# Kernel optimization log

Measured on AMD Instinct MI355X. Metric: run time of the kernel, lower is better.

## Reference

```python
import jax, jax.numpy as jnp
import numpy as np

B, I, O, S, C = 64, 2048, 2048, 10, 512  # batch, input, output, dendritic segments, context dim


def setup_inputs() -> dict:
    key = jax.random.key(0)
    ks = jax.random.split(key, 8)
    x = jax.random.normal(ks[0], (B, I), dtype=jnp.float32)
    context = jax.random.normal(ks[1], (B, C), dtype=jnp.float32)
    prev_activation = jax.random.normal(ks[2], (B, I), dtype=jnp.float32)
    # sparse-initialized weight: randn/sqrt(I) * (rand > sparsity)
    w = jax.random.normal(ks[3], (O, I), dtype=jnp.float32) / np.sqrt(I)
    mask = (jax.random.uniform(ks[4], (O, I)) > 0.9).astype(jnp.float32)
    weight = w * mask
    bias = jnp.zeros((O,), dtype=jnp.float32)
    astrocyte_activation = jnp.ones((O,), dtype=jnp.float32)
    astrocyte_threshold = jnp.full((O,), 0.5, dtype=jnp.float32)
    dendrite_segments = jax.random.normal(ks[5], (O, I, S), dtype=jnp.float32) / np.sqrt(I)
    dendritic_gates = jnp.ones((O, S), dtype=jnp.float32)
    connection_strength = jnp.ones((O, I), dtype=jnp.float32)
    pruning_threshold = jnp.full((1,), 0.01, dtype=jnp.float32)
    return {
        "x": x, "context": context, "prev_activation": prev_activation,
        "weight": weight, "bias": bias,
        "astrocyte_activation": astrocyte_activation,
        "astrocyte_threshold": astrocyte_threshold,
        "dendrite_segments": dendrite_segments,
        "dendritic_gates": dendritic_gates,
        "connection_strength": connection_strength,
        "pruning_threshold": pruning_threshold,
    }


def reference(x, context, prev_activation, weight, bias, astrocyte_activation,
              astrocyte_threshold, dendrite_segments, dendritic_gates,
              connection_strength, pruning_threshold):
    dt = x.dtype
    # structural plasticity (eval branch): prune weak connections
    conn_mask = (jnp.abs(weight) * connection_strength > pruning_threshold[0]).astype(dt)
    eff_w = weight * conn_mask  # [O, I]
    # astrocyte modulation
    ctx_signal = jnp.mean(context, axis=-1, keepdims=True)          # [B, 1]
    astro = jax.nn.sigmoid(ctx_signal * astrocyte_activation[None, :])  # [B, O]
    astro = astro * (astro > astrocyte_threshold[None, :]).astype(dt)
    mean_astro = jnp.mean(astro, axis=0)                            # [O]
    mod_w = eff_w * mean_astro[:, None]                             # [O, I]
    synaptic = x @ mod_w.T + bias                                   # [B, O]
    # multi-compartment dendritic processing
    seg_act = jnp.einsum('bi,ois->bos', x, dendrite_segments)       # [B, O, S]
    gated = jax.nn.relu(seg_act) * jax.nn.sigmoid(dendritic_gates)[None, :, :]
    dendritic = jnp.sum(gated, axis=-1)                             # [B, O]
    return jax.nn.relu(synaptic + dendritic)
```

## Files before the change

kernel.cpp:

```cpp
#include <hip/hip_runtime.h>
#include <math.h>

#define Bn 64
#define In 2048
#define On 2048
#define Sn 10
#define Cn 512

#define OT 4
#define KSPLIT 4
#define KRANGE (In / KSPLIT)
#define KT 128
#define NSTG (KRANGE / KT)
#define LROW 136
#define SLOT 12

typedef short short8 __attribute__((ext_vector_type(8)));
typedef float f32x4 __attribute__((ext_vector_type(4)));
typedef unsigned short ushort4v __attribute__((ext_vector_type(4)));

__device__ __forceinline__ unsigned short f2bf(float f) {
    union { float f; unsigned u; } v; v.f = f;
    unsigned r = (v.u + 0x7FFFu + ((v.u >> 16) & 1u)) >> 16;
    return (unsigned short)r;
}

__global__ void prep_kernel(const float* __restrict__ x,
                            const float* __restrict__ ctx,
                            float* __restrict__ ws_ctx,
                            unsigned short* __restrict__ ws_xbf) {
    const int b = blockIdx.x;
    const int t = threadIdx.x;
    if (b < Bn) {
        __shared__ float red[256];
        red[t] = ctx[b * Cn + t] + ctx[b * Cn + t + 256];
        __syncthreads();
        for (int off = 128; off > 0; off >>= 1) {
            if (t < off) red[t] += red[t + off];
            __syncthreads();
        }
        if (t == 0) ws_ctx[b] = red[0] * (1.0f / (float)Cn);
    } else {
        int idx = (b - Bn) * 256 + t;
        ws_xbf[idx] = f2bf(x[idx]);
    }
}

__global__ void mastro_kernel(const float* __restrict__ aact,
                              const float* __restrict__ athr,
                              const float* __restrict__ ws_ctx,
                              float* __restrict__ ws_mastro) {
    const int o = blockIdx.x * 256 + threadIdx.x;
    const float aa = aact[o], th = athr[o];
    float sum = 0.0f;
    for (int b = 0; b < Bn; ++b) {
        float sg = 1.0f / (1.0f + expf(-ws_ctx[b] * aa));
        if (sg > th) sum += sg;
    }
    ws_mastro[o] = sum * (1.0f / (float)Bn);
}

__global__ __launch_bounds__(256, 8)
void main_kernel(const unsigned short* __restrict__ xbf,
                 const float* __restrict__ wgt,
                 const float* __restrict__ cst,
                 const float* __restrict__ seg,
                 const float* __restrict__ prn,
                 float* __restrict__ P) {
    __shared__ __align__(16) unsigned short Blds[48 * LROW];

    const int t = threadIdx.x;
    const int grp = blockIdx.x >> 2;
    const int ks  = blockIdx.x & 3;
    const int o0 = grp * OT;
    const int ib = ks * KRANGE;
    const int w = t >> 6, l = t & 63;
    const int l15 = l & 15, q = l >> 4;
    const float pthr = prn[0];

    for (int idx = t; idx < 4 * LROW; idx += 256) Blds[44 * LROW + idx] = 0;

    f32x4 acc[3];
#pragma unroll
    for (int n = 0; n < 3; ++n) acc[n] = (f32x4){0.f, 0.f, 0.f, 0.f};

    const float* segw = seg + ((size_t)(o0 + w) * In) * Sn;

    for (int is = 0; is < NSTG; ++is) {
        const int i0 = ib + is * KT;

        unsigned psv[10];
        {
            const float* sp = segw + (size_t)i0 * Sn;
#pragma unroll
            for (int c = 0; c < 10; ++c) {
                float2 f2 = *(const float2*)(sp + c * 128 + 2 * l);
                psv[c] = (unsigned)f2bf(f2.x) | ((unsigned)f2bf(f2.y) << 16);
            }
        }
        ushort4v ew[2];
        if (w == 0) {
#pragma unroll
            for (int i = 0; i < 2; ++i) {
                const int o_l = i * 2 + (l >> 5);
                const int col = (l & 31) * 4;
                f32x4 wv = *(const f32x4*)(wgt + (size_t)(o0 + o_l) * In + i0 + col);
                f32x4 cv = *(const f32x4*)(cst + (size_t)(o0 + o_l) * In + i0 + col);
#pragma unroll
                for (int j = 0; j < 4; ++j) {
                    float wj = wv[j];
                    ew[i][j] = f2bf((__builtin_fabsf(wj) * cv[j] > pthr) ? wj : 0.0f);
                }
            }
        }

        __syncthreads();

#pragma unroll
        for (int c = 0; c < 10; ++c) {
            unsigned j = (unsigned)(c * 128 + 2 * l);
            unsigned ii = j / 10u;
            unsigned s = j - ii * 10u;
            unsigned short* bp = &Blds[(w * Sn + s) * LROW + ii];
            bp[0] = (unsigned short)psv[c];
            bp[LROW] = (unsigned short)(psv[c] >> 16);
        }
        if (w == 0) {
#pragma unroll
            for (int i = 0; i < 2; ++i) {
                const int o_l = i * 2 + (l >> 5);
                const int col = (l & 31) * 4;
                *(ushort4v*)&Blds[(40 + o_l) * LROW + col] = ew[i];
            }
        }
        __syncthreads();

        const unsigned short* xrow = xbf + (size_t)(w * 16 + l15) * In + i0 + q * 8;
#pragma unroll
        for (int kk = 0; kk < KT; kk += 32) {
            short8 a  = *(const short8*)(xrow + kk);
            short8 b0 = *(const short8*)&Blds[(0  + l15) * LROW + q * 8 + kk];
            short8 b1 = *(const short8*)&Blds[(16 + l15) * LROW + q * 8 + kk];
            short8 b2 = *(const short8*)&Blds[(32 + l15) * LROW + q * 8 + kk];
            acc[0] = __builtin_amdgcn_mfma_f32_16x16x32_bf16(a, b0, acc[0], 0, 0, 0);
            acc[1] = __builtin_amdgcn_mfma_f32_16x16x32_bf16(a, b1, acc[1], 0, 0, 0);
            acc[2] = __builtin_amdgcn_mfma_f32_16x16x32_bf16(a, b2, acc[2], 0, 0, 0);
        }
    }

#pragma unroll
    for (int nt = 0; nt < 3; ++nt) {
        const unsigned n = nt * 16 + l15;
#pragma unroll
        for (int r = 0; r < 4; ++r) {
            const int m = w * 16 + q * 4 + r;
            const size_t base = (((size_t)ks * Bn + m) * On + o0) * SLOT;
            if (n < 40u) {
                unsigned ol = n / 10u, s = n - ol * 10u;
                P[base + ol * SLOT + s] = acc[nt][r];
            } else if (n < 44u) {
                P[base + (n - 40u) * SLOT + 10] = acc[nt][r];
            }
        }
    }
}

__global__ void finalize_kernel(const float* __restrict__ P,
                                const float* __restrict__ gates,
                                const float* __restrict__ bias,
                                const float* __restrict__ ws_mastro,
                                float* __restrict__ out) {
    const int t = threadIdx.x;
    const int o = (blockIdx.x & 31) * 64 + (t & 63);
    const int b = (blockIdx.x >> 5) * 4 + (t >> 6);
    f32x4 v0 = {0.f, 0.f, 0.f, 0.f}, v1 = v0, v2 = v0;
#pragma unroll
    for (int ks = 0; ks < KSPLIT; ++ks) {
        const f32x4* p = (const f32x4*)(P + (((size_t)ks * Bn + b) * On + o) * SLOT);
        v0 += p[0]; v1 += p[1]; v2 += p[2];
    }
    float d[12];
#pragma unroll
    for (int j = 0; j < 4; ++j) { d[j] = v0[j]; d[4 + j] = v1[j]; d[8 + j] = v2[j]; }
    float dend = 0.0f;
#pragma unroll
    for (int s = 0; s < Sn; ++s) {
        float g = 1.0f / (1.0f + expf(-gates[o * Sn + s]));
        float r = d[s] > 0.0f ? d[s] : 0.0f;
        dend += r * g;
    }
    float val = d[10] * ws_mastro[o] + bias[o] + dend;
    out[(size_t)b * On + o] = val > 0.0f ? val : 0.0f;
}

extern "C" void kernel_launch(void* const* d_in, const int* in_sizes, int n_in,
                              void* d_out, int out_size, void* d_ws, size_t ws_size,
                              hipStream_t stream) {
    (void)in_sizes; (void)n_in; (void)out_size; (void)ws_size;
    const float* x    = (const float*)d_in[0];
    const float* ctx  = (const float*)d_in[1];
    const float* wgt  = (const float*)d_in[3];
    const float* bias = (const float*)d_in[4];
    const float* aact = (const float*)d_in[5];
    const float* athr = (const float*)d_in[6];
    const float* seg  = (const float*)d_in[7];
    const float* gat  = (const float*)d_in[8];
    const float* cst  = (const float*)d_in[9];
    const float* prn  = (const float*)d_in[10];
    float* out = (float*)d_out;

    float* ws_ctx = (float*)d_ws;
    unsigned short* ws_xbf = (unsigned short*)((char*)d_ws + 256);
    float* ws_mastro = (float*)((char*)d_ws + 262400);
    float* ws_P = (float*)((char*)d_ws + 270592);

    prep_kernel<<<Bn + (Bn * In) / 256, 256, 0, stream>>>(x, ctx, ws_ctx, ws_xbf);
    mastro_kernel<<<On / 256, 256, 0, stream>>>(aact, athr, ws_ctx, ws_mastro);
    main_kernel<<<(On / OT) * KSPLIT, 256, 0, stream>>>(ws_xbf, wgt, cst, seg, prn, ws_P);
    finalize_kernel<<<(On / 64) * (Bn / 4), 256, 0, stream>>>(ws_P, gat, bias, ws_mastro, out);
}
```

Baseline: 312.2 us.

## Double-buffer LDS stages with smaller K tile and vectorize partial-sum stores

Halves the K tile and double-buffers the shared-memory B tile so global loads for the next stage are issued while the current stage's MFMAs run. This removes one barrier per stage. The weight and connection-strength loads are spread across all four waves instead of only wave 0. The epilogue now stages the accumulators through LDS so each thread writes contiguous 16-byte vectors to the partial buffer instead of scattered scalar stores. In exchange it uses more LDS and has more loop iterations, each with less work.

```diff
diff --git a/kernel.cpp b/kernel.cpp
--- a/kernel.cpp
+++ b/kernel.cpp
@@ -10,14 +10,13 @@
 #define OT 4
 #define KSPLIT 4
 #define KRANGE (In / KSPLIT)
-#define KT 128
+#define KT 64
 #define NSTG (KRANGE / KT)
-#define LROW 136
+#define LROW 72
 #define SLOT 12
 
 typedef short short8 __attribute__((ext_vector_type(8)));
 typedef float f32x4 __attribute__((ext_vector_type(4)));
-typedef unsigned short ushort4v __attribute__((ext_vector_type(4)));
 
 __device__ __forceinline__ unsigned short f2bf(float f) {
     union { float f; unsigned u; } v; v.f = f;
@@ -67,7 +66,7 @@
                  const float* __restrict__ seg,
                  const float* __restrict__ prn,
                  float* __restrict__ P) {
-    __shared__ __align__(16) unsigned short Blds[48 * LROW];
+    __shared__ __align__(16) unsigned short Blds[2][48 * LROW];
 
     const int t = threadIdx.x;
     const int grp = blockIdx.x >> 2;
@@ -78,90 +77,99 @@
     const int l15 = l & 15, q = l >> 4;
     const float pthr = prn[0];
 
-    for (int idx = t; idx < 4 * LROW; idx += 256) Blds[44 * LROW + idx] = 0;
+    for (int idx = t; idx < 4 * LROW; idx += 256) {
+        Blds[0][44 * LROW + idx] = 0;
+        Blds[1][44 * LROW + idx] = 0;
+    }
+
+    const int ii0 = (2 * l) / 10;
+    const int s0  = (2 * l) % 10;
+
+    float2 sv[5];
+    float wv, cv;
+
+    const float* segw = seg + (size_t)(o0 + w) * In * Sn;
+
+    auto load_stage = [&](int is) {
+        const float* sp = segw + (size_t)(ib + is * KT) * Sn + 2 * l;
+#pragma unroll
+        for (int c = 0; c < 5; ++c) sv[c] = *(const float2*)(sp + c * 128);
+        wv = wgt[(size_t)(o0 + w) * In + ib + is * KT + l];
+        cv = cst[(size_t)(o0 + w) * In + ib + is * KT + l];
+    };
+
+    auto store_stage = [&](int bb) {
+        int ii = ii0, s = s0;
+#pragma unroll
+        for (int c = 0; c < 5; ++c) {
+            unsigned short* bp = &Blds[bb][(w * Sn + s) * LROW + ii];
+            bp[0]    = f2bf(sv[c].x);
+            bp[LROW] = f2bf(sv[c].y);
+            s += 8; ii += 12;
+            if (s >= 10) { s -= 10; ++ii; }
+        }
+        float e = (__builtin_fabsf(wv) * cv > pthr) ? wv : 0.0f;
+        Blds[bb][(40 + w) * LROW + l] = f2bf(e);
+    };
 
     f32x4 acc[3];
 #pragma unroll
     for (int n = 0; n < 3; ++n) acc[n] = (f32x4){0.f, 0.f, 0.f, 0.f};
 
-    const float* segw = seg + ((size_t)(o0 + w) * In) * Sn;
-
-    for (int is = 0; is < NSTG; ++is) {
-        const int i0 = ib + is * KT;
-
-        unsigned psv[10];
-        {
-            const float* sp = segw + (size_t)i0 * Sn;
-#pragma unroll
-            for (int c = 0; c < 10; ++c) {
-                float2 f2 = *(const float2*)(sp + c * 128 + 2 * l);
-                psv[c] = (unsigned)f2bf(f2.x) | ((unsigned)f2bf(f2.y) << 16);
-            }
-        }
-        ushort4v ew[2];
-        if (w == 0) {
-#pragma unroll
-            for (int i = 0; i < 2; ++i) {
-                const int o_l = i * 2 + (l >> 5);
-                const int col = (l & 31) * 4;
-                f32x4 wv = *(const f32x4*)(wgt + (size_t)(o0 + o_l) * In + i0 + col);
-                f32x4 cv = *(const f32x4*)(cst + (size_t)(o0 + o_l) * In + i0 + col);
-#pragma unroll
-                for (int j = 0; j < 4; ++j) {
-                    float wj = wv[j];
-                    ew[i][j] = f2bf((__builtin_fabsf(wj) * cv[j] > pthr) ? wj : 0.0f);
-                }
-            }
-        }
-
-        __syncthreads();
-
-#pragma unroll
-        for (int c = 0; c < 10; ++c) {
-            unsigned j = (unsigned)(c * 128 + 2 * l);
-            unsigned ii = j / 10u;
-            unsigned s = j - ii * 10u;
-            unsigned short* bp = &Blds[(w * Sn + s) * LROW + ii];
-            bp[0] = (unsigned short)psv[c];
-            bp[LROW] = (unsigned short)(psv[c] >> 16);
-        }
-        if (w == 0) {
-#pragma unroll
-            for (int i = 0; i < 2; ++i) {
-                const int o_l = i * 2 + (l >> 5);
-                const int col = (l & 31) * 4;
-                *(ushort4v*)&Blds[(40 + o_l) * LROW + col] = ew[i];
-            }
-        }
-        __syncthreads();
-
-        const unsigned short* xrow = xbf + (size_t)(w * 16 + l15) * In + i0 + q * 8;
+    auto compute = [&](int bb, int is) {
+        const unsigned short* xrow =
+            xbf + (size_t)(w * 16 + l15) * In + ib + is * KT + q * 8;
 #pragma unroll
         for (int kk = 0; kk < KT; kk += 32) {
             short8 a  = *(const short8*)(xrow + kk);
-            short8 b0 = *(const short8*)&Blds[(0  + l15) * LROW + q * 8 + kk];
-            short8 b1 = *(const short8*)&Blds[(16 + l15) * LROW + q * 8 + kk];
-            short8 b2 = *(const short8*)&Blds[(32 + l15) * LROW + q * 8 + kk];
+            short8 b0 = *(const short8*)&Blds[bb][(0  + l15) * LROW + q * 8 + kk];
+            short8 b1 = *(const short8*)&Blds[bb][(16 + l15) * LROW + q * 8 + kk];
+            short8 b2 = *(const short8*)&Blds[bb][(32 + l15) * LROW + q * 8 + kk];
             acc[0] = __builtin_amdgcn_mfma_f32_16x16x32_bf16(a, b0, acc[0], 0, 0, 0);
             acc[1] = __builtin_amdgcn_mfma_f32_16x16x32_bf16(a, b1, acc[1], 0, 0, 0);
             acc[2] = __builtin_amdgcn_mfma_f32_16x16x32_bf16(a, b2, acc[2], 0, 0, 0);
         }
-    }
-
+    };
+
+    load_stage(0);
+    store_stage(0);
+    load_stage(1);
+    __syncthreads();
+    for (int is = 0; is < NSTG; ++is) {
+        compute(is & 1, is);
+        if (is + 1 < NSTG) {
+            store_stage((is + 1) & 1);
+            if (is + 2 < NSTG) load_stage(is + 2);
+        }
+        __syncthreads();
+    }
+
+    float* scratch = (float*)&Blds[0][0] + w * (16 * 48);
 #pragma unroll
     for (int nt = 0; nt < 3; ++nt) {
-        const unsigned n = nt * 16 + l15;
-#pragma unroll
-        for (int r = 0; r < 4; ++r) {
-            const int m = w * 16 + q * 4 + r;
-            const size_t base = (((size_t)ks * Bn + m) * On + o0) * SLOT;
-            if (n < 40u) {
-                unsigned ol = n / 10u, s = n - ol * 10u;
-                P[base + ol * SLOT + s] = acc[nt][r];
-            } else if (n < 44u) {
-                P[base + (n - 40u) * SLOT + 10] = acc[nt][r];
-            }
-        }
+        const int n = nt * 16 + l15;
+        if (n < 44) {
+#pragma unroll
+            for (int r = 0; r < 4; ++r)
+                scratch[(q * 4 + r) * 48 + n] = acc[nt][r];
+        }
+    }
+    __syncthreads();
+    {
+        const int mloc = l >> 2, ol = l & 3;
+        const float* srow = (const float*)&Blds[0][0] + w * (16 * 48) + mloc * 48;
+        float d[10];
+#pragma unroll
+        for (int s = 0; s < 10; ++s) d[s] = srow[ol * 10 + s];
+        const float syn = srow[40 + ol];
+        f32x4 p0 = {d[0], d[1], d[2], d[3]};
+        f32x4 p1 = {d[4], d[5], d[6], d[7]};
+        f32x4 p2 = {d[8], d[9], syn, 0.0f};
+        const int m = w * 16 + mloc;
+        float* pp = P + (((size_t)ks * Bn + m) * On + o0 + ol) * SLOT;
+        *(f32x4*)(pp)     = p0;
+        *(f32x4*)(pp + 4) = p1;
+        *(f32x4*)(pp + 8) = p2;
     }
 }
 
```

Result: faster. 301.2 us (-3.5%).
